# Optimization experiments

Measured on AMD Instinct MI355X. Metric: run time of the kernel, lower is better.

## Reference

```python
import jax, jax.numpy as jnp
import numpy as np
from jax import lax

B, CI, CO, H, W, K, RANK, SR = 8, 64, 64, 256, 256, 3, 4, 1
SHIFTS = [(dy, dx) for dy in range(-SR, SR + 1) for dx in range(-SR, SR + 1)]  # 9 shifts
N_PAIRS = len(SHIFTS) * (len(SHIFTS) + 1) // 2  # 45 unordered pairs (j >= i)


def conv3x3(x, w, b):
    # torch Conv2d == cross-correlation, 'SAME' padding for odd kernel
    y = lax.conv_general_dilated(x, w, window_strides=(1, 1), padding='SAME',
                                 dimension_numbers=('NCHW', 'OIHW', 'NCHW'))
    return y + b[None, :, None, None]


def setup_inputs() -> dict:
    key = jax.random.key(0)
    ks = jax.random.split(key, 7)
    return {
        'x': jax.random.normal(ks[0], (B, CI, H, W), jnp.float32) * 0.5,
        'linear_w': jax.random.normal(ks[1], (CO, CI, K, K), jnp.float32) * 0.05,
        'linear_b': jax.random.normal(ks[2], (CO,), jnp.float32) * 0.05,
        'w2a_w': jax.random.normal(ks[3], (RANK, CO, CI), jnp.float32) * 0.05,
        'w2a_b': jax.random.normal(ks[4], (RANK, CO), jnp.float32) * 0.05,
        'w2b_w': jax.random.normal(ks[5], (RANK, CO, CO), jnp.float32) * 0.05,
        'w2b_b': jax.random.normal(ks[6], (RANK, CO), jnp.float32) * 0.05,
    }


def reference(x, linear_w, linear_b, w2a_w, w2a_b, w2b_w, w2b_b):
    # Linear Volterra term: 3x3 conv
    F1 = conv3x3(x, linear_w, linear_b)

    # Quadratic term. Original loops over 45 shift pairs (i <= j) computing
    # prod = Xi*Xj and pushing each through the rank-q 1x1 convs. Since the
    # 1x1 convs are affine, (1/P) * sum_pairs Wb(Wa(prod)) == Wb(Wa(S/P))
    # where S = sum_{i<=j} Xi*Xj. And S = ((sum_i Xi)^2 + sum_i Xi^2) / 2.
    sum_x = jnp.zeros_like(x)
    sum_x2 = jnp.zeros_like(x)
    x2 = x * x
    for (dy, dx) in SHIFTS:  # fixed structural loop over 9 circular shifts
        sum_x = sum_x + jnp.roll(x, (dy, dx), axis=(2, 3))
        sum_x2 = sum_x2 + jnp.roll(x2, (dy, dx), axis=(2, 3))
    S = 0.5 * (sum_x * sum_x + sum_x2)  # [B, CI, H, W]
    Sn = S / N_PAIRS

    F2 = jnp.zeros_like(F1)
    for q in range(RANK):  # fixed small rank loop
        h = jnp.einsum('oi,bihw->bohw', w2a_w[q], Sn) + w2a_b[q][None, :, None, None]
        F2 = F2 + jnp.einsum('oi,bihw->bohw', w2b_w[q], h) + w2b_b[q][None, :, None, None]

    return F1 + F2
```

## Files before the change

kernel.cpp:

```cpp
#include <hip/hip_runtime.h>

#define NB 8
#define NC 64
#define NH 256
#define NW 256

typedef short s16x8 __attribute__((ext_vector_type(8)));
typedef float f32x16 __attribute__((ext_vector_type(16)));

static __device__ __forceinline__ unsigned short f2bf(float f) {
  unsigned int u = __float_as_uint(f);
  unsigned int r = (u + 0x7fffu + ((u >> 16) & 1u)) >> 16;
  return (unsigned short)r;
}

#define WS_NEEDED 134299904ull

__global__ __launch_bounds__(256) void prep_fast(
    const float* __restrict__ lw, const float* __restrict__ lb,
    const float* __restrict__ w2a_w, const float* __restrict__ w2a_b,
    const float* __restrict__ w2b_w, const float* __restrict__ w2b_b,
    unsigned short* __restrict__ Wg, float* __restrict__ bias) {
  int blk = blockIdx.x;
  int t = threadIdx.x;
  if (blk < 16) {
    int gidx = blk * 256 + t;
    int ci = gidx & 63, co = gidx >> 6;
    float acc = 0.f;
    for (int q = 0; q < 4; ++q) {
      const float* wb = w2b_w + (q * 64 + co) * 64;
      const float* wa = w2a_w + q * 4096 + ci;
      for (int c = 0; c < 64; ++c) acc += wb[c] * wa[c * 64];
    }
    Wg[9 * 4096 + co * 64 + ci] = f2bf(acc * (1.0f / 90.0f));
    return;
  }
  for (int idx = (blk - 16) * 256 + t; idx < 64 * 64 * 9; idx += 48 * 256) {
    int ci = idx & 63;
    int co = (idx >> 6) & 63;
    int tap = idx >> 12;
    Wg[idx] = f2bf(lw[(co * 64 + ci) * 9 + tap]);
  }
  if (blk == 16 && t < 64) {
    float acc = lb[t];
    for (int q = 0; q < 4; ++q) {
      const float* wb = w2b_w + (q * 64 + t) * 64;
      const float* ba = w2a_b + q * 64;
      for (int c = 0; c < 64; ++c) acc += wb[c] * ba[c];
      acc += w2b_b[q * 64 + t];
    }
    bias[t] = acc;
  }
}

__global__ __launch_bounds__(512, 4) void stage1(
    const float* __restrict__ x, unsigned short* __restrict__ xT,
    unsigned short* __restrict__ snT) {
  __shared__ __align__(16) unsigned short xb[NW * 64];
  __shared__ __align__(16) unsigned short sb[NW * 64];
  int id = blockIdx.x;
  int bid = (id & 7) * 256 + (id >> 3);
  int b = bid >> 8, h = bid & 255;
  int tid = threadIdx.x;
  int w = tid & 255;
  int ciBase = (tid >> 8) * 32;
  int hm = (h + 255) & 255, hp = (h + 1) & 255;
  int wm = (w + 255) & 255, wp = (w + 1) & 255;
  const float* xbase = x + (size_t)b * 64 * 65536;
  char* xbc = (char*)xb;
  char* sbc = (char*)sb;
  int swz = (w & 7) << 4;
  int rowm = hm * 256, row0 = h * 256, rowp = hp * 256;
  for (int i = 0; i < 16; ++i) {
    int ci = ciBase + i * 2;
    const float* p0 = xbase + (size_t)ci * 65536;
    const float* p1 = p0 + 65536;
    float a0 = p0[rowm + wm], a1 = p0[rowm + w], a2 = p0[rowm + wp];
    float b0 = p0[row0 + wm], b1 = p0[row0 + w], b2 = p0[row0 + wp];
    float c0 = p0[rowp + wm], c1 = p0[rowp + w], c2 = p0[rowp + wp];
    float d0 = p1[rowm + wm], d1 = p1[rowm + w], d2 = p1[rowm + wp];
    float e0 = p1[row0 + wm], e1 = p1[row0 + w], e2 = p1[row0 + wp];
    float f0 = p1[rowp + wm], f1 = p1[rowp + w], f2 = p1[rowp + wp];
    float u0 = a0 + a1 + a2 + b0 + b1 + b2 + c0 + c1 + c2;
    float v0 = a0 * a0 + a1 * a1 + a2 * a2 + b0 * b0 + b1 * b1 + b2 * b2 +
               c0 * c0 + c1 * c1 + c2 * c2;
    float u1 = d0 + d1 + d2 + e0 + e1 + e2 + f0 + f1 + f2;
    float v1 = d0 * d0 + d1 * d1 + d2 * d2 + e0 * e0 + e1 * e1 + e2 * e2 +
               f0 * f0 + f1 * f1 + f2 * f2;
    float sn0 = u0 * u0 + v0;
    float sn1 = u1 * u1 + v1;
    unsigned int xp = (unsigned int)f2bf(b1) | ((unsigned int)f2bf(e1) << 16);
    unsigned int sp = (unsigned int)f2bf(sn0) | ((unsigned int)f2bf(sn1) << 16);
    int off = (w * 128 + ci * 2) ^ swz;
    *(unsigned int*)(xbc + off) = xp;
    *(unsigned int*)(sbc + off) = sp;
  }
  __syncthreads();
  int r = tid >> 3, c = tid & 7;
  size_t gbase = ((size_t)(b * 256 + h) * 256) * 128;
#pragma unroll
  for (int pass = 0; pass < 4; ++pass) {
    int rr = r + pass * 64;
    int loff = (rr * 128 + c * 16) ^ ((rr & 7) << 4);
    float4 vx = *(float4*)(xbc + loff);
    float4 vs = *(float4*)(sbc + loff);
    *(float4*)((char*)xT + gbase + rr * 128 + c * 16) = vx;
    *(float4*)((char*)snT + gbase + rr * 128 + c * 16) = vs;
  }
}

#define XH_OFF 0
#define SN_OFF 19008
#define WL_OFF 31296
#define LDS_SZ 51776

__global__ __launch_bounds__(256, 3) void stage2(
    const unsigned short* __restrict__ xT, const unsigned short* __restrict__ snT,
    const unsigned short* __restrict__ Wg, const float* __restrict__ bias,
    float* __restrict__ out) {
  __shared__ __align__(16) char smem[LDS_SZ];
  int id = blockIdx.x;
  int bid = (id & 7) * 256 + (id >> 3);
  int b = bid >> 8;
  int rem = bid & 255;
  int h0 = (rem >> 2) * 4, w0 = (rem & 3) * 64;
  int tid = threadIdx.x;
  int lane = tid & 63, wv = tid >> 6;
  int l31 = lane & 31, g = lane >> 5;

  f32x16 acc[2][2];
#pragma unroll
  for (int m = 0; m < 2; ++m)
#pragma unroll
    for (int n = 0; n < 2; ++n)
#pragma unroll
      for (int i = 0; i < 16; ++i) acc[m][n][i] = 0.f;

  for (int ck = 0; ck < 4; ++ck) {
    int ci0 = ck * 16;
    __syncthreads();
    for (int idx = tid; idx < 792; idx += 256) {
      int row = idx >> 1, half = idx & 1;
      int hr = row / 66, wc = row - hr * 66;
      int gh = h0 - 1 + hr, gw = w0 - 1 + wc;
      float4 v = make_float4(0.f, 0.f, 0.f, 0.f);
      if ((unsigned)gh < 256u && (unsigned)gw < 256u)
        v = *(const float4*)((const char*)xT +
              (((size_t)(b * 256 + gh) * 256 + gw) * 64 + ci0 + half * 8) * 2);
      *(float4*)(smem + XH_OFF + row * 48 + half * 16) = v;
    }
    for (int idx = tid; idx < 512; idx += 256) {
      int row = idx >> 1, half = idx & 1;
      int ph = row >> 6, pw = row & 63;
      float4 v = *(const float4*)((const char*)snT +
            (((size_t)(b * 256 + h0 + ph) * 256 + w0 + pw) * 64 + ci0 + half * 8) * 2);
      *(float4*)(smem + SN_OFF + row * 48 + half * 16) = v;
    }
    for (int idx = tid; idx < 1280; idx += 256) {
      int s = idx >> 7;
      int m = (idx >> 6) & 1;
      int l = idx & 63;
      float4 v = *(const float4*)((const char*)Wg +
            ((size_t)(s * 64 + m * 32 + (l & 31)) * 64 + ci0 + (l >> 5) * 8) * 2);
      *(float4*)(smem + WL_OFF + idx * 16) = v;
    }
    __syncthreads();

#pragma unroll
    for (int s = 0; s < 10; ++s) {
      s16x8 af[2], bf[2];
#pragma unroll
      for (int m = 0; m < 2; ++m)
        af[m] = *(const s16x8*)(smem + WL_OFF + ((s * 2 + m) * 64 + lane) * 16);
      if (s < 9) {
        const int dy = s / 3, dx = s - dy * 3;
        int rbase = ((wv + dy) * 66 + l31 + dx) * 48 + g * 16;
#pragma unroll
        for (int n = 0; n < 2; ++n)
          bf[n] = *(const s16x8*)(smem + XH_OFF + rbase + n * 32 * 48);
      } else {
        int rbase = (wv * 64 + l31) * 48 + g * 16;
#pragma unroll
        for (int n = 0; n < 2; ++n)
          bf[n] = *(const s16x8*)(smem + SN_OFF + rbase + n * 32 * 48);
      }
#pragma unroll
      for (int m = 0; m < 2; ++m)
#pragma unroll
        for (int n = 0; n < 2; ++n)
          acc[m][n] = __builtin_amdgcn_mfma_f32_32x32x16_bf16(af[m], bf[n],
                                                              acc[m][n], 0, 0, 0);
    }
  }

  int h = h0 + wv;
#pragma unroll
  for (int m = 0; m < 2; ++m) {
#pragma unroll
    for (int reg = 0; reg < 16; ++reg) {
      int co = m * 32 + (reg & 3) + 8 * (reg >> 2) + 4 * (lane >> 5);
      float bv = bias[co];
#pragma unroll
      for (int n = 0; n < 2; ++n) {
        int w = w0 + n * 32 + l31;
        out[(((size_t)b * 64 + co) * 256 + h) * 256 + w] = acc[m][n][reg] + bv;
      }
    }
  }
}

#define TW 128
#define CC 16

__global__ __launch_bounds__(256) void prep_kernel(
    const float* __restrict__ lw, const float* __restrict__ w2a_w,
    const float* __restrict__ w2a_b, const float* __restrict__ w2b_w,
    const float* __restrict__ w2b_b, float* __restrict__ Mt,
    float* __restrict__ bias2, float* __restrict__ Wt) {
  int t = threadIdx.x;
  for (int idx = t; idx < NC * NC; idx += 256) {
    int i = idx >> 6, o = idx & 63;
    float acc = 0.f;
    for (int q = 0; q < 4; ++q) {
      const float* wb = w2b_w + (q * NC + o) * NC;
      const float* wa = w2a_w + q * NC * NC + i;
      for (int c = 0; c < NC; ++c) acc += wb[c] * wa[c * NC];
    }
    Mt[idx] = acc;
  }
  if (t < NC) {
    float acc = 0.f;
    for (int q = 0; q < 4; ++q) {
      const float* wb = w2b_w + (q * NC + t) * NC;
      const float* ba = w2a_b + q * NC;
      for (int c = 0; c < NC; ++c) acc += wb[c] * ba[c];
      acc += w2b_b[q * NC + t];
    }
    bias2[t] = acc;
  }
  for (int idx = t; idx < NC * 9 * NC; idx += 256) {
    int co = idx & 63;
    int tap = (idx >> 6) % 9;
    int ci = idx / (9 * 64);
    Wt[idx] = lw[(co * NC + ci) * 9 + tap];
  }
}

__global__ __launch_bounds__(256) void volterra_main(
    const float* __restrict__ x, const float* __restrict__ lb,
    const float* __restrict__ Mt, const float* __restrict__ bias2,
    const float* __restrict__ Wt, float* __restrict__ out) {
  __shared__ __align__(16) float xt[CC][3][TW + 8];
  __shared__ __align__(16) float snt[CC][TW];
  const int tid = threadIdx.x;
  const int wc = blockIdx.x;
  const int h = blockIdx.y;
  const int b = blockIdx.z;
  const int w0 = wc * TW;
  const int co = tid >> 2;
  const int wq = tid & 3;
  const int wl0 = wq * 32;
  const bool fix_lo = (w0 == 0) && (wq == 0);
  const bool fix_hi = (w0 + TW == NW) && (wq == 3);
  float acc[32];
  {
    float base = lb[co] + bias2[co];
#pragma unroll
    for (int k = 0; k < 32; ++k) acc[k] = base;
  }
  for (int cc = 0; cc < NC / CC; ++cc) {
    const int ci0 = cc * CC;
    __syncthreads();
    for (int idx = tid; idx < CC * 3 * (TW + 2); idx += 256) {
      int col = idx % (TW + 2);
      int rem = idx / (TW + 2);
      int dy = rem % 3;
      int ci = rem / 3;
      int gr = (h + dy - 1 + NH) & (NH - 1);
      int gc = (w0 - 1 + col + NW) & (NW - 1);
      xt[ci][dy][col] = x[(((size_t)b * NC + ci0 + ci) * NH + gr) * NW + gc];
    }
    __syncthreads();
    for (int idx = tid; idx < CC * TW; idx += 256) {
      int ci = idx >> 7, wl = idx & (TW - 1);
      float s1 = 0.f, s2 = 0.f;
#pragma unroll
      for (int dy = 0; dy < 3; ++dy)
#pragma unroll
        for (int dx = 0; dx < 3; ++dx) {
          float v = xt[ci][dy][wl + dx];
          s1 += v;
          s2 += v * v;
        }
      snt[ci][wl] = (s1 * s1 + s2) * (0.5f / 45.0f);
    }
    __syncthreads();
    for (int ci = 0; ci < CC; ++ci) {
      const int cig = ci0 + ci;
      {
        float m = Mt[cig * NC + co];
        const float4* sp = reinterpret_cast<const float4*>(&snt[ci][wl0]);
#pragma unroll
        for (int j = 0; j < 8; ++j) {
          float4 v = sp[j];
          acc[4 * j + 0] += m * v.x;
          acc[4 * j + 1] += m * v.y;
          acc[4 * j + 2] += m * v.z;
          acc[4 * j + 3] += m * v.w;
        }
      }
      const float* wtp = Wt + cig * 9 * NC + co;
#pragma unroll
      for (int dy = 0; dy < 3; ++dy) {
        if (dy == 0 && h == 0) continue;
        if (dy == 2 && h == NH - 1) continue;
        float wv0 = wtp[(dy * 3 + 0) * NC];
        float wv1 = wtp[(dy * 3 + 1) * NC];
        float wv2 = wtp[(dy * 3 + 2) * NC];
        float xr[34];
        const float4* rp = reinterpret_cast<const float4*>(&xt[ci][dy][wl0]);
#pragma unroll
        for (int j = 0; j < 8; ++j) {
          float4 v = rp[j];
          xr[4 * j + 0] = v.x;
          xr[4 * j + 1] = v.y;
          xr[4 * j + 2] = v.z;
          xr[4 * j + 3] = v.w;
        }
        xr[32] = xt[ci][dy][wl0 + 32];
        xr[33] = xt[ci][dy][wl0 + 33];
        if (fix_lo) xr[0] = 0.f;
        if (fix_hi) xr[33] = 0.f;
#pragma unroll
        for (int k = 0; k < 32; ++k) {
          acc[k] += wv0 * xr[k] + wv1 * xr[k + 1] + wv2 * xr[k + 2];
        }
      }
    }
  }
  float* op = out + (((size_t)b * NC + co) * NH + h) * NW + w0 + wl0;
#pragma unroll
  for (int j = 0; j < 8; ++j) {
    float4 v;
    v.x = acc[4 * j + 0];
    v.y = acc[4 * j + 1];
    v.z = acc[4 * j + 2];
    v.w = acc[4 * j + 3];
    reinterpret_cast<float4*>(op)[j] = v;
  }
}

extern "C" void kernel_launch(void* const* d_in, const int* in_sizes, int n_in,
                              void* d_out, int out_size, void* d_ws, size_t ws_size,
                              hipStream_t stream) {
  const float* x = (const float*)d_in[0];
  const float* lw = (const float*)d_in[1];
  const float* lb = (const float*)d_in[2];
  const float* w2a_w = (const float*)d_in[3];
  const float* w2a_b = (const float*)d_in[4];
  const float* w2b_w = (const float*)d_in[5];
  const float* w2b_b = (const float*)d_in[6];
  float* out = (float*)d_out;

  if (ws_size >= WS_NEEDED) {
    char* ws = (char*)d_ws;
    unsigned short* xT = (unsigned short*)(ws);
    unsigned short* snT = (unsigned short*)(ws + 67108864);
    unsigned short* Wg = (unsigned short*)(ws + 134217728);
    float* bias = (float*)(ws + 134299648);
    prep_fast<<<64, 256, 0, stream>>>(lw, lb, w2a_w, w2a_b, w2b_w, w2b_b, Wg, bias);
    stage1<<<2048, 512, 0, stream>>>(x, xT, snT);
    stage2<<<2048, 256, 0, stream>>>(xT, snT, Wg, bias, out);
  } else {
    float* ws = (float*)d_ws;
    float* Mt = ws;
    float* bias2 = ws + 4096;
    float* Wt = ws + 4096 + 64;
    prep_kernel<<<1, 256, 0, stream>>>(lw, w2a_w, w2a_b, w2b_w, w2b_b, Mt, bias2, Wt);
    dim3 grid(NW / TW, NH, NB);
    volterra_main<<<grid, 256, 0, stream>>>(x, lb, Mt, bias2, Wt, out);
  }
}
```

Measured before the change: 395.5 us.

## Store intermediates channel-chunk-major and pre-swizzle weights into LDS fragment order

The bf16 intermediates xT and snT are now written as four planes of 16 channels each, instead of 64 interleaved channels per pixel. Each stage2 chunk load then reads a contiguous 32-byte record per pixel rather than a strided 32-byte piece of a 128-byte record. The combined weights are pre-arranged by prep_fast into the exact per-chunk, per-tap MFMA fragment order, so stage2 copies them with plain linear 16-byte loads. The aim is better coalescing and less address arithmetic in the global-to-LDS loads. Stage1 stores become scattered across four planes in exchange.

Measured after the change: 365.9 us. 7.5% less time.

```diff
diff --git a/kernel.cpp b/kernel.cpp
--- a/kernel.cpp
+++ b/kernel.cpp
@@ -15,12 +15,20 @@
 }
 
 #define WS_NEEDED 134299904ull
+#define CKSTRIDE 16777216ull
+
+static __device__ __forceinline__ int wfoff(int tap, int co, int ci) {
+  int ck = ci >> 4;
+  int lane = (((ci >> 3) & 1) << 5) | (co & 31);
+  int m = co >> 5;
+  return ((((ck * 10 + tap) * 2 + m) * 64 + lane) << 3) | (ci & 7);
+}
 
 __global__ __launch_bounds__(256) void prep_fast(
     const float* __restrict__ lw, const float* __restrict__ lb,
     const float* __restrict__ w2a_w, const float* __restrict__ w2a_b,
     const float* __restrict__ w2b_w, const float* __restrict__ w2b_b,
-    unsigned short* __restrict__ Wg, float* __restrict__ bias) {
+    unsigned short* __restrict__ Wf, float* __restrict__ bias) {
   int blk = blockIdx.x;
   int t = threadIdx.x;
   if (blk < 16) {
@@ -32,14 +40,14 @@
       const float* wa = w2a_w + q * 4096 + ci;
       for (int c = 0; c < 64; ++c) acc += wb[c] * wa[c * 64];
     }
-    Wg[9 * 4096 + co * 64 + ci] = f2bf(acc * (1.0f / 90.0f));
+    Wf[wfoff(9, co, ci)] = f2bf(acc * (1.0f / 90.0f));
     return;
   }
   for (int idx = (blk - 16) * 256 + t; idx < 64 * 64 * 9; idx += 48 * 256) {
     int ci = idx & 63;
     int co = (idx >> 6) & 63;
     int tap = idx >> 12;
-    Wg[idx] = f2bf(lw[(co * 64 + ci) * 9 + tap]);
+    Wf[wfoff(tap, co, ci)] = f2bf(lw[(co * 64 + ci) * 9 + tap]);
   }
   if (blk == 16 && t < 64) {
     float acc = lb[t];
@@ -97,15 +105,18 @@
   }
   __syncthreads();
   int r = tid >> 3, c = tid & 7;
-  size_t gbase = ((size_t)(b * 256 + h) * 256) * 128;
+  int ck = c >> 1, half = c & 1;
+  size_t pbase = (size_t)b * 65536 + (size_t)h * 256;
+  char* xdst = (char*)xT + (size_t)ck * CKSTRIDE + half * 16;
+  char* sdst = (char*)snT + (size_t)ck * CKSTRIDE + half * 16;
 #pragma unroll
   for (int pass = 0; pass < 4; ++pass) {
     int rr = r + pass * 64;
     int loff = (rr * 128 + c * 16) ^ ((rr & 7) << 4);
     float4 vx = *(float4*)(xbc + loff);
     float4 vs = *(float4*)(sbc + loff);
-    *(float4*)((char*)xT + gbase + rr * 128 + c * 16) = vx;
-    *(float4*)((char*)snT + gbase + rr * 128 + c * 16) = vs;
+    *(float4*)(xdst + (pbase + rr) * 32) = vx;
+    *(float4*)(sdst + (pbase + rr) * 32) = vs;
   }
 }
 
@@ -116,7 +127,7 @@
 
 __global__ __launch_bounds__(256, 3) void stage2(
     const unsigned short* __restrict__ xT, const unsigned short* __restrict__ snT,
-    const unsigned short* __restrict__ Wg, const float* __restrict__ bias,
+    const unsigned short* __restrict__ Wf, const float* __restrict__ bias,
     float* __restrict__ out) {
   __shared__ __align__(16) char smem[LDS_SZ];
   int id = blockIdx.x;
@@ -137,7 +148,9 @@
       for (int i = 0; i < 16; ++i) acc[m][n][i] = 0.f;
 
   for (int ck = 0; ck < 4; ++ck) {
-    int ci0 = ck * 16;
+    const char* xsrc = (const char*)xT + (size_t)ck * CKSTRIDE;
+    const char* ssrc = (const char*)snT + (size_t)ck * CKSTRIDE;
+    const char* wsrc = (const char*)Wf + ck * 20480;
     __syncthreads();
     for (int idx = tid; idx < 792; idx += 256) {
       int row = idx >> 1, half = idx & 1;
@@ -145,23 +158,19 @@
       int gh = h0 - 1 + hr, gw = w0 - 1 + wc;
       float4 v = make_float4(0.f, 0.f, 0.f, 0.f);
       if ((unsigned)gh < 256u && (unsigned)gw < 256u)
-        v = *(const float4*)((const char*)xT +
-              (((size_t)(b * 256 + gh) * 256 + gw) * 64 + ci0 + half * 8) * 2);
+        v = *(const float4*)(xsrc +
+              ((size_t)b * 65536 + gh * 256 + gw) * 32 + half * 16);
       *(float4*)(smem + XH_OFF + row * 48 + half * 16) = v;
     }
     for (int idx = tid; idx < 512; idx += 256) {
       int row = idx >> 1, half = idx & 1;
       int ph = row >> 6, pw = row & 63;
-      float4 v = *(const float4*)((const char*)snT +
-            (((size_t)(b * 256 + h0 + ph) * 256 + w0 + pw) * 64 + ci0 + half * 8) * 2);
+      float4 v = *(const float4*)(ssrc +
+            ((size_t)b * 65536 + (h0 + ph) * 256 + w0 + pw) * 32 + half * 16);
       *(float4*)(smem + SN_OFF + row * 48 + half * 16) = v;
     }
     for (int idx = tid; idx < 1280; idx += 256) {
-      int s = idx >> 7;
-      int m = (idx >> 6) & 1;
-      int l = idx & 63;
-      float4 v = *(const float4*)((const char*)Wg +
-            ((size_t)(s * 64 + m * 32 + (l & 31)) * 64 + ci0 + (l >> 5) * 8) * 2);
+      float4 v = *(const float4*)(wsrc + idx * 16);
       *(float4*)(smem + WL_OFF + idx * 16) = v;
     }
     __syncthreads();
@@ -366,11 +375,11 @@
     char* ws = (char*)d_ws;
     unsigned short* xT = (unsigned short*)(ws);
     unsigned short* snT = (unsigned short*)(ws + 67108864);
-    unsigned short* Wg = (unsigned short*)(ws + 134217728);
+    unsigned short* Wf = (unsigned short*)(ws + 134217728);
     float* bias = (float*)(ws + 134299648);
-    prep_fast<<<64, 256, 0, stream>>>(lw, lb, w2a_w, w2a_b, w2b_w, w2b_b, Wg, bias);
+    prep_fast<<<64, 256, 0, stream>>>(lw, lb, w2a_w, w2a_b, w2b_w, w2b_b, Wf, bias);
     stage1<<<2048, 512, 0, stream>>>(x, xT, snT);
-    stage2<<<2048, 256, 0, stream>>>(xT, snT, Wg, bias, out);
+    stage2<<<2048, 256, 0, stream>>>(xT, snT, Wf, bias, out);
   } else {
     float* ws = (float*)d_ws;
     float* Mt = ws;
```
